# Kernel optimization log

Measured on AMD Instinct MI355X. Metric: run time of the kernel, lower is better.

The kernel has to match this reference:

```python
import jax, jax.numpy as jnp
import numpy as np

# NF4 codebook (bitsandbytes normal-float-4 quantiles)
NF4_CODE = jnp.array([
    -1.0, -0.6961928009986877, -0.5250730514526367, -0.39491748809814453,
    -0.28444138169288635, -0.18477343022823334, -0.09105003625154495, 0.0,
    0.07958029955625534, 0.16093020141124725, 0.24611230194568634, 0.33791524171829224,
    0.44070982933044434, 0.5626170039176941, 0.7229568362236023, 1.0
], dtype=jnp.float32)

BLOCK = 64  # bitsandbytes default quantization block size


def setup_inputs() -> dict:
    key = jax.random.key(0)
    k1, k2, k3 = jax.random.split(key, 3)
    B, S, IN, OUT = 4, 2048, 4096, 16384
    x = jax.random.normal(k1, (B, S, IN), dtype=jnp.float32)
    w_codes = jax.random.randint(k2, (OUT, IN), 0, 16, dtype=jnp.int32)
    absmax = jax.random.uniform(k3, (OUT, IN // BLOCK), dtype=jnp.float32)
    return {"x": x, "w_codes": w_codes, "absmax": absmax}


def reference(x, w_codes, absmax):
    OUT, IN = w_codes.shape
    # dequantize: codebook lookup then per-block scale (NF4 blockwise dequant)
    w = NF4_CODE[w_codes].reshape(OUT, IN // BLOCK, BLOCK) * absmax[:, :, None]
    w = w.reshape(OUT, IN)  # [out, in] dequantized weight
    # F.linear(x, w): y = x @ w.T
    return jnp.einsum('bsi,oi->bso', x, w)
```

## Files before the change

### kernel.cpp

```cpp
#include <hip/hip_runtime.h>

#define M_DIM 8192
#define N_DIM 16384
#define K_DIM 4096
#define QBLK  64

#define BM 256
#define BN 256
#define IBK 128
#define INT_TILES (K_DIM / IBK)

typedef short  s8v  __attribute__((ext_vector_type(8)));
typedef unsigned short u16x8 __attribute__((ext_vector_type(8)));
typedef float  f4v  __attribute__((ext_vector_type(4)));
typedef int    i4v  __attribute__((ext_vector_type(4)));

__constant__ float NF4C[16] = {
    -1.0f, -0.6961928009986877f, -0.5250730514526367f, -0.39491748809814453f,
    -0.28444138169288635f, -0.18477343022823334f, -0.09105003625154495f, 0.0f,
    0.07958029955625534f, 0.16093020141124725f, 0.24611230194568634f, 0.33791524171829224f,
    0.44070982933044434f, 0.5626170039176941f, 0.7229568362236023f, 1.0f
};

__device__ __forceinline__ unsigned short f2bf(float f) {
    union { float f; unsigned u; } v; v.f = f;
    unsigned r = v.u + 0x7FFFu + ((v.u >> 16) & 1u);
    return (unsigned short)(r >> 16);
}

__device__ __forceinline__ void async16(const void* g, void* l) {
    __builtin_amdgcn_global_load_lds(
        (const __attribute__((address_space(1))) void*)g,
        (__attribute__((address_space(3))) void*)l,
        16, 0, 0);
}

#define WAITVM(n)  asm volatile("s_waitcnt vmcnt(" #n ")" ::: "memory")
#define BARX()     asm volatile("s_barrier" ::: "memory")
#define PRIO1      __builtin_amdgcn_s_setprio(1)
#define PRIO0      __builtin_amdgcn_s_setprio(0)

__global__ void quant_x_kernel(const float* __restrict__ x,
                               signed char* __restrict__ xq,
                               float* __restrict__ sx) {
    const int m = blockIdx.x, t = threadIdx.x;
    const int lane = t & 63, wv = t >> 6;
    const float4* px = (const float4*)(x + (size_t)m * K_DIM + t * 16);
    float4 v0 = px[0], v1 = px[1], v2 = px[2], v3 = px[3];
    float amax = 0.f;
#define AB4(v) amax = fmaxf(amax, fmaxf(fmaxf(fabsf(v.x), fabsf(v.y)), fmaxf(fabsf(v.z), fabsf(v.w))));
    AB4(v0) AB4(v1) AB4(v2) AB4(v3)
#undef AB4
    for (int off = 32; off; off >>= 1) amax = fmaxf(amax, __shfl_xor(amax, off));
    __shared__ float red[4];
    if (lane == 0) red[wv] = amax;
    __syncthreads();
    amax = fmaxf(fmaxf(red[0], red[1]), fmaxf(red[2], red[3]));
    const float inv = (amax > 0.f) ? 127.0f / amax : 0.f;
    if (t == 0) sx[m] = amax * (1.0f / 127.0f);
    int4 o;
#define PK(a,b,c,d) ((__float2int_rn((a)*inv)&255)|((__float2int_rn((b)*inv)&255)<<8)|\
                     ((__float2int_rn((c)*inv)&255)<<16)|((__float2int_rn((d)*inv)&255)<<24))
    o.x = PK(v0.x, v0.y, v0.z, v0.w);
    o.y = PK(v1.x, v1.y, v1.z, v1.w);
    o.z = PK(v2.x, v2.y, v2.z, v2.w);
    o.w = PK(v3.x, v3.y, v3.z, v3.w);
#undef PK
    *(int4*)(xq + (size_t)m * K_DIM + t * 16) = o;
}

__global__ void quant_w_kernel(const int* __restrict__ codes,
                               const float* __restrict__ am,
                               signed char* __restrict__ wq,
                               float* __restrict__ sw) {
    __shared__ float lut[16];
    __shared__ float red[4];
    const int o = blockIdx.x, t = threadIdx.x;
    const int lane = t & 63, wv = t >> 6;
    if (t < 16) lut[t] = NF4C[t];
    const float ab = am[o * (K_DIM / QBLK) + (t >> 2)];
    float amax = ab;
    for (int off = 32; off; off >>= 1) amax = fmaxf(amax, __shfl_xor(amax, off));
    if (lane == 0) red[wv] = amax;
    __syncthreads();
    amax = fmaxf(fmaxf(red[0], red[1]), fmaxf(red[2], red[3]));
    const float inv = (amax > 0.f) ? 127.0f / amax : 0.f;
    if (t == 0) sw[o] = amax * (1.0f / 127.0f);
    const int4* pc = (const int4*)(codes + (size_t)o * K_DIM + t * 16);
    int4 c0 = pc[0], c1 = pc[1], c2 = pc[2], c3 = pc[3];
    const float s = ab * inv;
    int4 oo;
#define PKW(q) (__float2int_rn(lut[q] * s) & 255)
    oo.x = PKW(c0.x) | (PKW(c0.y) << 8) | (PKW(c0.z) << 16) | (PKW(c0.w) << 24);
    oo.y = PKW(c1.x) | (PKW(c1.y) << 8) | (PKW(c1.z) << 16) | (PKW(c1.w) << 24);
    oo.z = PKW(c2.x) | (PKW(c2.y) << 8) | (PKW(c2.z) << 16) | (PKW(c2.w) << 24);
    oo.w = PKW(c3.x) | (PKW(c3.y) << 8) | (PKW(c3.z) << 16) | (PKW(c3.w) << 24);
#undef PKW
    *(int4*)(wq + (size_t)o * K_DIM + t * 16) = oo;
}

__global__ __launch_bounds__(512, 2)
void gemm_i8_kernel(const signed char* __restrict__ A,
                    const signed char* __restrict__ B,
                    const float* __restrict__ sx,
                    const float* __restrict__ sw,
                    float* __restrict__ Cp) {
    __shared__ __attribute__((aligned(16))) unsigned char lds[131072];

    const int tid  = threadIdx.x;
    const int wid  = tid >> 6;
    const int lane = tid & 63;
    const int wm   = wid >> 2;
    const int wn   = wid & 3;

    const int bid = blockIdx.x;
    const int wg  = (bid & 7) * 256 + (bid >> 3);
    const int bm0 = (wg >> 6) * BM;
    const int bn0 = (wg & 63) * BN;

    const int scol = (((tid & 7) ^ ((tid >> 3) & 7)) << 4);
    int Rr[2];
    Rr[0] = tid >> 3;
    Rr[1] = 64 + (tid >> 3);

    const signed char* pA0[2]; const signed char* pA1[2];
    const signed char* pB0[2]; const signed char* pB1[2];
#pragma unroll
    for (int i = 0; i < 2; ++i) {
        pA0[i] = A + (size_t)(bm0 + Rr[i]) * K_DIM + scol;
        pA1[i] = pA0[i] + (size_t)128 * K_DIM;
        pB0[i] = B + (size_t)(bn0 + Rr[i]) * K_DIM + scol;
        pB1[i] = pB0[i] + (size_t)128 * K_DIM;
    }

#define STG(R, P, KO)                                                         \
    { unsigned char* d = lds + (R) * 16384 + wid * 1024;                      \
      async16(P[0] + (KO), d);                                                \
      async16(P[1] + (KO), d + 8192); }

    const int fr = lane & 15, kg = lane >> 4;
    const int qL0 = fr * 128 + ((kg * 16) ^ ((fr & 7) << 4));
    const int qL1 = qL0 ^ 64;
    const char* ldsc = (const char*)lds;

    i4v acc[8][4];
#pragma unroll
    for (int i = 0; i < 8; ++i)
#pragma unroll
        for (int j = 0; j < 4; ++j) acc[i][j] = i4v{0, 0, 0, 0};

    i4v aset[4][2], b0set[2][2], b1set[2][2];

#define RD_A(R)                                                               \
    { const char* ba = ldsc + (R) * 16384 + wm * 8192;                        \
      _Pragma("unroll") for (int fm = 0; fm < 4; ++fm) {                      \
          aset[fm][0] = *(const i4v*)(ba + fm * 2048 + qL0);                  \
          aset[fm][1] = *(const i4v*)(ba + fm * 2048 + qL1); } }

#define RD_B(R, BS)                                                           \
    { const char* bb = ldsc + (R) * 16384 + wn * 4096;                        \
      _Pragma("unroll") for (int fn = 0; fn < 2; ++fn) {                      \
          BS[fn][0] = *(const i4v*)(bb + fn * 2048 + qL0);                    \
          BS[fn][1] = *(const i4v*)(bb + fn * 2048 + qL1); } }

#define MM(qm, qn, BS)                                                        \
    _Pragma("unroll") for (int kk = 0; kk < 2; ++kk)                          \
      _Pragma("unroll") for (int fm = 0; fm < 4; ++fm)                        \
        _Pragma("unroll") for (int fn = 0; fn < 2; ++fn)                      \
          acc[(qm)*4+fm][(qn)*2+fn] = __builtin_amdgcn_mfma_i32_16x16x64_i8(  \
            aset[fm][kk], BS[fn][kk], acc[(qm)*4+fm][(qn)*2+fn], 0, 0, 0);

    STG(0, pA0, 0); STG(2, pB0, 0); STG(3, pB1, 0); STG(1, pA1, 0);
    WAITVM(0);
    BARX();

    for (int t = 0; t < INT_TILES - 1; ++t) {
        const int b4 = (t & 1) * 4;
        const int o4 = 4 - b4;
        const int kn = (t + 1) * IBK;

        RD_A(b4 + 0); RD_B(b4 + 2, b0set);
        STG(o4 + 0, pA0, kn);
        PRIO1; MM(0, 0, b0set); PRIO0;
        WAITVM(4); BARX();

        RD_B(b4 + 3, b1set);
        STG(o4 + 2, pB0, kn);
        PRIO1; MM(0, 1, b1set); PRIO0;
        WAITVM(4); BARX();

        RD_A(b4 + 1);
        STG(o4 + 3, pB1, kn);
        PRIO1; MM(1, 1, b1set); PRIO0;
        STG(o4 + 1, pA1, kn);
        PRIO1; MM(1, 0, b0set); PRIO0;
        WAITVM(4); BARX();
    }

    {
        const int b4 = ((INT_TILES - 1) & 1) * 4;
        RD_A(b4 + 0); RD_B(b4 + 2, b0set);
        PRIO1; MM(0, 0, b0set); PRIO0;
        WAITVM(2); BARX();
        RD_B(b4 + 3, b1set);
        PRIO1; MM(0, 1, b1set); PRIO0;
        WAITVM(0); BARX();
        RD_A(b4 + 1);
        PRIO1; MM(1, 1, b1set); MM(1, 0, b0set); PRIO0;
    }

#pragma unroll
    for (int m8 = 0; m8 < 8; ++m8) {
        const int grow = bm0 + (m8 >> 2) * 128 + wm * 64 + (m8 & 3) * 16 + (lane >> 4) * 4;
        float sxr[4];
#pragma unroll
        for (int r = 0; r < 4; ++r) sxr[r] = sx[grow + r];
#pragma unroll
        for (int n4 = 0; n4 < 4; ++n4) {
            const int gcol = bn0 + (n4 >> 1) * 128 + wn * 32 + (n4 & 1) * 16 + (lane & 15);
            const float swc = sw[gcol];
            float* yp = Cp + (size_t)grow * N_DIM + gcol;
#pragma unroll
            for (int r = 0; r < 4; ++r)
                yp[(size_t)r * N_DIM] = sxr[r] * swc * (float)acc[m8][n4][r];
        }
    }
#undef STG
#undef RD_A
#undef RD_B
#undef MM
}

__global__ void gemm_fused_kernel(const float* __restrict__ X,
                                  const int* __restrict__ W,
                                  const float* __restrict__ am,
                                  float* __restrict__ C) {
    __shared__ __attribute__((aligned(16))) unsigned short ldsA[128 * 32];
    __shared__ __attribute__((aligned(16))) unsigned short ldsB[128 * 32];
    __shared__ float lut[16];

    const int tid = threadIdx.x;
    if (tid < 16) lut[tid] = NF4C[tid];
    __syncthreads();

    const int wave = tid >> 6, lane = tid & 63;
    const int wr = wave >> 1, wc = wave & 1;
    const int bid = blockIdx.x;
    const int wg  = (bid & 7) * 1024 + (bid >> 3);
    const int bm0 = (wg >> 7) * 128;
    const int bn0 = (wg & 127) * 128;

    const int row = tid >> 2, col8 = (tid & 3) * 8;
    const float* gX0 = X + (size_t)(bm0 + row) * K_DIM + col8;
    const float* gX1 = gX0 + (size_t)64 * K_DIM;
    const int*   gW0 = W + (size_t)(bn0 + row) * K_DIM + col8;
    const int*   gW1 = gW0 + (size_t)64 * K_DIM;
    const int amRow0 = (bn0 + row) * (K_DIM / QBLK);
    const int amRow1 = (bn0 + row + 64) * (K_DIM / QBLK);

    unsigned short* sA0 = ldsA + tid * 8;
    unsigned short* sA1 = ldsA + (tid + 256) * 8;
    unsigned short* sB0 = ldsB + tid * 8;
    unsigned short* sB1 = ldsB + (tid + 256) * 8;

    f4v acc[4][4];
#pragma unroll
    for (int i = 0; i < 4; ++i)
#pragma unroll
        for (int j = 0; j < 4; ++j) acc[i][j] = f4v{0.f, 0.f, 0.f, 0.f};

    const int fr = lane & 15, kg = lane >> 4;
    const unsigned short* pa = ldsA + (wr * 64 + fr) * 32 + kg * 8;
    const unsigned short* pb = ldsB + (wc * 64 + fr) * 32 + kg * 8;

    for (int k0 = 0; k0 < K_DIM; k0 += 32) {
        float4 x0a = *(const float4*)(gX0 + k0);
        float4 x0b = *(const float4*)(gX0 + k0 + 4);
        float4 x1a = *(const float4*)(gX1 + k0);
        float4 x1b = *(const float4*)(gX1 + k0 + 4);
        int4 w0a = *(const int4*)(gW0 + k0);
        int4 w0b = *(const int4*)(gW0 + k0 + 4);
        int4 w1a = *(const int4*)(gW1 + k0);
        int4 w1b = *(const int4*)(gW1 + k0 + 4);
        float s0 = am[amRow0 + ((k0 + col8) >> 6)];
        float s1 = am[amRow1 + ((k0 + col8) >> 6)];

        u16x8 A0, A1, B0, B1;
        A0[0] = f2bf(x0a.x); A0[1] = f2bf(x0a.y); A0[2] = f2bf(x0a.z); A0[3] = f2bf(x0a.w);
        A0[4] = f2bf(x0b.x); A0[5] = f2bf(x0b.y); A0[6] = f2bf(x0b.z); A0[7] = f2bf(x0b.w);
        A1[0] = f2bf(x1a.x); A1[1] = f2bf(x1a.y); A1[2] = f2bf(x1a.z); A1[3] = f2bf(x1a.w);
        A1[4] = f2bf(x1b.x); A1[5] = f2bf(x1b.y); A1[6] = f2bf(x1b.z); A1[7] = f2bf(x1b.w);
        B0[0] = f2bf(lut[w0a.x] * s0); B0[1] = f2bf(lut[w0a.y] * s0);
        B0[2] = f2bf(lut[w0a.z] * s0); B0[3] = f2bf(lut[w0a.w] * s0);
        B0[4] = f2bf(lut[w0b.x] * s0); B0[5] = f2bf(lut[w0b.y] * s0);
        B0[6] = f2bf(lut[w0b.z] * s0); B0[7] = f2bf(lut[w0b.w] * s0);
        B1[0] = f2bf(lut[w1a.x] * s1); B1[1] = f2bf(lut[w1a.y] * s1);
        B1[2] = f2bf(lut[w1a.z] * s1); B1[3] = f2bf(lut[w1a.w] * s1);
        B1[4] = f2bf(lut[w1b.x] * s1); B1[5] = f2bf(lut[w1b.y] * s1);
        B1[6] = f2bf(lut[w1b.z] * s1); B1[7] = f2bf(lut[w1b.w] * s1);

        __syncthreads();
        *(u16x8*)sA0 = A0; *(u16x8*)sA1 = A1;
        *(u16x8*)sB0 = B0; *(u16x8*)sB1 = B1;
        __syncthreads();

        s8v a[4], b[4];
#pragma unroll
        for (int i = 0; i < 4; ++i) a[i] = *(const s8v*)(pa + i * 16 * 32);
#pragma unroll
        for (int i = 0; i < 4; ++i) b[i] = *(const s8v*)(pb + i * 16 * 32);
#pragma unroll
        for (int i = 0; i < 4; ++i)
#pragma unroll
            for (int j = 0; j < 4; ++j)
                acc[i][j] = __builtin_amdgcn_mfma_f32_16x16x32_bf16(a[i], b[j], acc[i][j], 0, 0, 0);
    }

    const int row0 = bm0 + wr * 64 + (lane >> 4) * 4;
    const int col0 = bn0 + wc * 64 + (lane & 15);
#pragma unroll
    for (int i = 0; i < 4; ++i)
#pragma unroll
        for (int j = 0; j < 4; ++j) {
            float* yp = C + (size_t)(row0 + i * 16) * N_DIM + col0 + j * 16;
#pragma unroll
            for (int r = 0; r < 4; ++r) yp[(size_t)r * N_DIM] = acc[i][j][r];
        }
}

extern "C" void kernel_launch(void* const* d_in, const int* in_sizes, int n_in,
                              void* d_out, int out_size, void* d_ws, size_t ws_size,
                              hipStream_t stream) {
    const float* x     = (const float*)d_in[0];
    const int*   codes = (const int*)d_in[1];
    const float* am    = (const float*)d_in[2];
    float* y = (float*)d_out;

    const size_t MK = (size_t)M_DIM * K_DIM;
    const size_t NK = (size_t)N_DIM * K_DIM;
    const size_t need = MK + NK + (M_DIM + N_DIM) * sizeof(float);

    if (ws_size >= need) {
        signed char* xq = (signed char*)d_ws;
        signed char* wq = xq + MK;
        float* sx = (float*)(wq + NK);
        float* sw = sx + M_DIM;
        quant_x_kernel<<<M_DIM, 256, 0, stream>>>(x, xq, sx);
        quant_w_kernel<<<N_DIM, 256, 0, stream>>>(codes, am, wq, sw);
        const int ngrid = (M_DIM / BM) * (N_DIM / BN);
        gemm_i8_kernel<<<ngrid, 512, 0, stream>>>(xq, wq, sx, sw, y);
    } else {
        const int ngrid = (M_DIM / 128) * (N_DIM / 128);
        gemm_fused_kernel<<<ngrid, 256, 0, stream>>>(x, codes, am, y);
    }
}
```

Measured before the change: 610.1 us.

## Shrink int8 GEMM tile to 128x128 with 4 waves and simple double buffering

Replaces the 256x256, 8-wave int8 GEMM with a 128x128, 4-wave kernel that keeps 64 KB of LDS and double-buffers whole A/B k-tiles. The old split into three phases per k-step, each with its own wait and barrier, becomes one phase: read A and B, issue the next tile's loads, run all MFMAs, then wait and sync. Smaller tiles give more workgroups and may allow more to fit per CU. The cost is roughly double the global and LDS traffic per MFMA and less overlap between loads and compute.

```diff
diff --git a/kernel.cpp b/kernel.cpp
--- a/kernel.cpp
+++ b/kernel.cpp
@@ -5,15 +5,15 @@
 #define K_DIM 4096
 #define QBLK  64
 
-#define BM 256
-#define BN 256
+#define BM 128
+#define BN 128
 #define IBK 128
 #define INT_TILES (K_DIM / IBK)
 
 typedef short  s8v  __attribute__((ext_vector_type(8)));
 typedef unsigned short u16x8 __attribute__((ext_vector_type(8)));
-typedef float  f4v  __attribute__((ext_vector_type(4)));
-typedef int    i4v  __attribute__((ext_vector_type(4)));
+typedef float  f4v   __attribute__((ext_vector_type(4)));
+typedef int    i4v   __attribute__((ext_vector_type(4)));
 
 __constant__ float NF4C[16] = {
     -1.0f, -0.6961928009986877f, -0.5250730514526367f, -0.39491748809814453f,
@@ -99,57 +99,47 @@
     *(int4*)(wq + (size_t)o * K_DIM + t * 16) = oo;
 }
 
-__global__ __launch_bounds__(512, 2)
-void gemm_i8_kernel(const signed char* __restrict__ A,
-                    const signed char* __restrict__ B,
-                    const float* __restrict__ sx,
-                    const float* __restrict__ sw,
-                    float* __restrict__ Cp) {
-    __shared__ __attribute__((aligned(16))) unsigned char lds[131072];
+__global__ __launch_bounds__(256, 2)
+void gemm_i8_2b_kernel(const signed char* __restrict__ A,
+                       const signed char* __restrict__ B,
+                       const float* __restrict__ sx,
+                       const float* __restrict__ sw,
+                       float* __restrict__ Cp) {
+    __shared__ __attribute__((aligned(16))) unsigned char lds[65536];
 
     const int tid  = threadIdx.x;
     const int wid  = tid >> 6;
     const int lane = tid & 63;
-    const int wm   = wid >> 2;
-    const int wn   = wid & 3;
+    const int wm   = wid >> 1;
+    const int wn   = wid & 1;
 
     const int bid = blockIdx.x;
-    const int wg  = (bid & 7) * 256 + (bid >> 3);
-    const int bm0 = (wg >> 6) * BM;
-    const int bn0 = (wg & 63) * BN;
+    const int wg  = (bid & 7) * 1024 + (bid >> 3);
+    const int bm0 = (wg >> 7) * BM;
+    const int bn0 = (wg & 127) * BN;
 
     const int scol = (((tid & 7) ^ ((tid >> 3) & 7)) << 4);
-    int Rr[2];
-    Rr[0] = tid >> 3;
-    Rr[1] = 64 + (tid >> 3);
-
-    const signed char* pA0[2]; const signed char* pA1[2];
-    const signed char* pB0[2]; const signed char* pB1[2];
-#pragma unroll
-    for (int i = 0; i < 2; ++i) {
-        pA0[i] = A + (size_t)(bm0 + Rr[i]) * K_DIM + scol;
-        pA1[i] = pA0[i] + (size_t)128 * K_DIM;
-        pB0[i] = B + (size_t)(bn0 + Rr[i]) * K_DIM + scol;
-        pB1[i] = pB0[i] + (size_t)128 * K_DIM;
-    }
+    const int srow = tid >> 3;
+    const signed char* pA = A + (size_t)(bm0 + srow) * K_DIM + scol;
+    const signed char* pB = B + (size_t)(bn0 + srow) * K_DIM + scol;
 
 #define STG(R, P, KO)                                                         \
-    { unsigned char* d = lds + (R) * 16384 + wid * 1024;                      \
-      async16(P[0] + (KO), d);                                                \
-      async16(P[1] + (KO), d + 8192); }
+    { _Pragma("unroll") for (int i = 0; i < 4; ++i)                           \
+        async16(P + (size_t)i * 32 * K_DIM + (KO),                            \
+                lds + (R) * 16384 + i * 4096 + wid * 1024); }
 
     const int fr = lane & 15, kg = lane >> 4;
     const int qL0 = fr * 128 + ((kg * 16) ^ ((fr & 7) << 4));
     const int qL1 = qL0 ^ 64;
     const char* ldsc = (const char*)lds;
 
-    i4v acc[8][4];
-#pragma unroll
-    for (int i = 0; i < 8; ++i)
+    i4v acc[4][4];
+#pragma unroll
+    for (int i = 0; i < 4; ++i)
 #pragma unroll
         for (int j = 0; j < 4; ++j) acc[i][j] = i4v{0, 0, 0, 0};
 
-    i4v aset[4][2], b0set[2][2], b1set[2][2];
+    i4v aset[4][2], bset[4][2];
 
 #define RD_A(R)                                                               \
     { const char* ba = ldsc + (R) * 16384 + wm * 8192;                        \
@@ -157,78 +147,61 @@
           aset[fm][0] = *(const i4v*)(ba + fm * 2048 + qL0);                  \
           aset[fm][1] = *(const i4v*)(ba + fm * 2048 + qL1); } }
 
-#define RD_B(R, BS)                                                           \
-    { const char* bb = ldsc + (R) * 16384 + wn * 4096;                        \
-      _Pragma("unroll") for (int fn = 0; fn < 2; ++fn) {                      \
-          BS[fn][0] = *(const i4v*)(bb + fn * 2048 + qL0);                    \
-          BS[fn][1] = *(const i4v*)(bb + fn * 2048 + qL1); } }
-
-#define MM(qm, qn, BS)                                                        \
+#define RD_B(R)                                                               \
+    { const char* bb = ldsc + (R) * 16384 + wn * 8192;                        \
+      _Pragma("unroll") for (int fn = 0; fn < 4; ++fn) {                      \
+          bset[fn][0] = *(const i4v*)(bb + fn * 2048 + qL0);                  \
+          bset[fn][1] = *(const i4v*)(bb + fn * 2048 + qL1); } }
+
+#define MMALL()                                                               \
     _Pragma("unroll") for (int kk = 0; kk < 2; ++kk)                          \
       _Pragma("unroll") for (int fm = 0; fm < 4; ++fm)                        \
-        _Pragma("unroll") for (int fn = 0; fn < 2; ++fn)                      \
-          acc[(qm)*4+fm][(qn)*2+fn] = __builtin_amdgcn_mfma_i32_16x16x64_i8(  \
-            aset[fm][kk], BS[fn][kk], acc[(qm)*4+fm][(qn)*2+fn], 0, 0, 0);
-
-    STG(0, pA0, 0); STG(2, pB0, 0); STG(3, pB1, 0); STG(1, pA1, 0);
+        _Pragma("unroll") for (int fn = 0; fn < 4; ++fn)                      \
+          acc[fm][fn] = __builtin_amdgcn_mfma_i32_16x16x64_i8(                \
+              aset[fm][kk], bset[fn][kk], acc[fm][fn], 0, 0, 0);
+
+    STG(0, pA, 0); STG(1, pB, 0);
     WAITVM(0);
     BARX();
 
     for (int t = 0; t < INT_TILES - 1; ++t) {
-        const int b4 = (t & 1) * 4;
-        const int o4 = 4 - b4;
+        const int rb = (t & 1) * 2;
+        const int ob = 2 - rb;
         const int kn = (t + 1) * IBK;
 
-        RD_A(b4 + 0); RD_B(b4 + 2, b0set);
-        STG(o4 + 0, pA0, kn);
-        PRIO1; MM(0, 0, b0set); PRIO0;
-        WAITVM(4); BARX();
-
-        RD_B(b4 + 3, b1set);
-        STG(o4 + 2, pB0, kn);
-        PRIO1; MM(0, 1, b1set); PRIO0;
-        WAITVM(4); BARX();
-
-        RD_A(b4 + 1);
-        STG(o4 + 3, pB1, kn);
-        PRIO1; MM(1, 1, b1set); PRIO0;
-        STG(o4 + 1, pA1, kn);
-        PRIO1; MM(1, 0, b0set); PRIO0;
-        WAITVM(4); BARX();
+        RD_A(rb + 0); RD_B(rb + 1);
+        STG(ob + 0, pA, kn);
+        STG(ob + 1, pB, kn);
+        PRIO1; MMALL(); PRIO0;
+        WAITVM(0); BARX();
     }
 
     {
-        const int b4 = ((INT_TILES - 1) & 1) * 4;
-        RD_A(b4 + 0); RD_B(b4 + 2, b0set);
-        PRIO1; MM(0, 0, b0set); PRIO0;
-        WAITVM(2); BARX();
-        RD_B(b4 + 3, b1set);
-        PRIO1; MM(0, 1, b1set); PRIO0;
-        WAITVM(0); BARX();
-        RD_A(b4 + 1);
-        PRIO1; MM(1, 1, b1set); MM(1, 0, b0set); PRIO0;
-    }
-
-#pragma unroll
-    for (int m8 = 0; m8 < 8; ++m8) {
-        const int grow = bm0 + (m8 >> 2) * 128 + wm * 64 + (m8 & 3) * 16 + (lane >> 4) * 4;
+        const int rb = ((INT_TILES - 1) & 1) * 2;
+        RD_A(rb + 0); RD_B(rb + 1);
+        PRIO1; MMALL(); PRIO0;
+    }
+
+#pragma unroll
+    for (int fm = 0; fm < 4; ++fm) {
+        const int grow = bm0 + wm * 64 + fm * 16 + (lane >> 4) * 4;
         float sxr[4];
 #pragma unroll
         for (int r = 0; r < 4; ++r) sxr[r] = sx[grow + r];
 #pragma unroll
-        for (int n4 = 0; n4 < 4; ++n4) {
-            const int gcol = bn0 + (n4 >> 1) * 128 + wn * 32 + (n4 & 1) * 16 + (lane & 15);
+        for (int fn = 0; fn < 4; ++fn) {
+            const int gcol = bn0 + wn * 64 + fn * 16 + (lane & 15);
             const float swc = sw[gcol];
             float* yp = Cp + (size_t)grow * N_DIM + gcol;
 #pragma unroll
             for (int r = 0; r < 4; ++r)
-                yp[(size_t)r * N_DIM] = sxr[r] * swc * (float)acc[m8][n4][r];
+                yp[(size_t)r * N_DIM] = sxr[r] * swc * (float)acc[fm][fn][r];
         }
     }
 #undef STG
 #undef RD_A
 #undef RD_B
-#undef MM
+#undef MMALL
 }
 
 __global__ void gemm_fused_kernel(const float* __restrict__ X,
@@ -348,7 +321,7 @@
         quant_x_kernel<<<M_DIM, 256, 0, stream>>>(x, xq, sx);
         quant_w_kernel<<<N_DIM, 256, 0, stream>>>(codes, am, wq, sw);
         const int ngrid = (M_DIM / BM) * (N_DIM / BN);
-        gemm_i8_kernel<<<ngrid, 512, 0, stream>>>(xq, wq, sx, sw, y);
+        gemm_i8_2b_kernel<<<ngrid, 256, 0, stream>>>(xq, wq, sx, sw, y);
     } else {
         const int ngrid = (M_DIM / 128) * (N_DIM / 128);
         gemm_fused_kernel<<<ngrid, 256, 0, stream>>>(x, codes, am, y);
```

Result: slower. 817.0 us (+33.9%).
